# Performance work log

Measured on AMD Instinct MI355X. Metric: run time of the kernel, lower is better.

## Reference

```python
import jax, jax.numpy as jnp
import numpy as np

N, D_IN, D_HID, D_OUT, E = 8192, 1024, 4096, 1024, 8

def setup_inputs() -> dict:
    key = jax.random.key(0)
    ks = jax.random.split(key, 5)
    s_in = 1.0 / np.sqrt(D_IN)
    s_hid = 1.0 / np.sqrt(D_HID)
    return {
        "x": jax.random.normal(ks[0], (N, D_IN), dtype=jnp.float32),
        "W1": jax.random.normal(ks[1], (E, D_IN, D_HID), dtype=jnp.float32) * s_in,
        "b1": jnp.zeros((E, D_HID), dtype=jnp.float32),
        "W2": jax.random.normal(ks[2], (E, D_HID, D_OUT), dtype=jnp.float32) * s_hid,
        "b2": jnp.zeros((E, D_OUT), dtype=jnp.float32),
        "Wg": jax.random.normal(ks[3], (D_IN, E), dtype=jnp.float32) * s_in,
        "bg": jnp.zeros((E,), dtype=jnp.float32),
        "k": 2,
    }

def reference(x, W1, b1, W2, b2, Wg, bg, k):
    # Gating: softmax over ALL experts, then mask to top-k and renormalize
    scores = x @ Wg + bg                      # [N, E]
    _, topk_idx = jax.lax.top_k(scores, k)    # [N, k]
    mask = jax.nn.one_hot(topk_idx, scores.shape[-1], dtype=scores.dtype).sum(-2)  # [N, E]
    w = jax.nn.softmax(scores, axis=-1) * mask
    w = w / (w.sum(-1, keepdims=True) + 1e-8)  # [N, E]
    # Dense compute-all-experts (faithful to torch.stack over experts)
    h = jax.nn.relu(jnp.einsum('ni,eih->enh', x, W1) + b1[:, None, :])  # [E, N, hid]
    outs = jnp.einsum('enh,eho->eno', h, W2) + b2[:, None, :]           # [E, N, out]
    # Weighted combine over experts
    return jnp.einsum('ne,eno->no', w, outs)   # [N, out]
```

## Files before the change

kernel.cpp:

```cpp
#include <hip/hip_runtime.h>
#include <hip/hip_bf16.h>
#include <stdint.h>

#define N_TOK 8192
#define DIN   1024
#define DHID  4096
#define DOUT  1024
#define NE    8

typedef __attribute__((ext_vector_type(8))) __bf16 bf16x8;
typedef __attribute__((ext_vector_type(4))) float  f32x4;
typedef __attribute__((ext_vector_type(8))) unsigned short u16x8;

__device__ __forceinline__ unsigned short f2bfu(float f) {
    union { float f; unsigned u; } a; a.f = f;
    unsigned r = a.u + 0x7FFF + ((a.u >> 16) & 1);
    return (unsigned short)(r >> 16);
}

__device__ __forceinline__ void gload_lds16(const void* g, void* l) {
    __builtin_amdgcn_global_load_lds(
        (__attribute__((address_space(1))) void*)(void*)g,
        (__attribute__((address_space(3))) void*)l,
        16, 0, 0);
}

__global__ void transpose_cast_kernel(const float* __restrict__ in, unsigned short* __restrict__ out,
                                      int R, int C) {
    __shared__ float t[64][65];
    const size_t RC = (size_t)R * C;
    const float* ine = in + (size_t)blockIdx.z * RC;
    unsigned short* oute = out + (size_t)blockIdx.z * RC;
    int c0 = blockIdx.x * 64, r0 = blockIdx.y * 64;
    int tid = threadIdx.x;
    #pragma unroll
    for (int it = 0; it < 4; it++) {
        int idx = it * 256 + tid;
        int r = idx >> 4, cq = (idx & 15) * 4;
        float4 v = *(const float4*)(ine + (size_t)(r0 + r) * C + c0 + cq);
        t[r][cq] = v.x; t[r][cq + 1] = v.y; t[r][cq + 2] = v.z; t[r][cq + 3] = v.w;
    }
    __syncthreads();
    #pragma unroll
    for (int it = 0; it < 2; it++) {
        int u = it * 256 + tid;
        int c = u >> 3, g = (u & 7) * 8;
        u16x8 o;
        #pragma unroll
        for (int v = 0; v < 8; v++) o[v] = f2bfu(t[g + v][c]);
        *(u16x8*)(oute + (size_t)(c0 + c) * R + r0 + g) = o;
    }
}

__global__ void gate_kernel(const float* __restrict__ x, const float* __restrict__ Wg,
                            const float* __restrict__ bg, int* __restrict__ counts,
                            int* __restrict__ tok_list, int* __restrict__ slot_list,
                            float* __restrict__ wslot, unsigned short* __restrict__ xb) {
    int wv = threadIdx.x >> 6, lane = threadIdx.x & 63;
    int n = blockIdx.x * 4 + wv;
    float acc[NE];
    #pragma unroll
    for (int e = 0; e < NE; e++) acc[e] = 0.f;
    const float* xr = x + (size_t)n * DIN;
    unsigned short* xbr = xb + (size_t)n * DIN;
    #pragma unroll
    for (int i = 0; i < DIN / 256; i++) {
        int d = i * 256 + lane * 4;
        float4 xv = *(const float4*)(xr + d);
        ushort4 o;
        o.x = f2bfu(xv.x); o.y = f2bfu(xv.y); o.z = f2bfu(xv.z); o.w = f2bfu(xv.w);
        *(ushort4*)(xbr + d) = o;
        const float* w = Wg + (size_t)d * NE;
        #pragma unroll
        for (int u = 0; u < 4; u++) {
            float xs = (&xv.x)[u];
            float4 w0 = *(const float4*)(w + u * NE);
            float4 w1 = *(const float4*)(w + u * NE + 4);
            acc[0] += xs * w0.x; acc[1] += xs * w0.y; acc[2] += xs * w0.z; acc[3] += xs * w0.w;
            acc[4] += xs * w1.x; acc[5] += xs * w1.y; acc[6] += xs * w1.z; acc[7] += xs * w1.w;
        }
    }
    #pragma unroll
    for (int off = 32; off; off >>= 1)
        #pragma unroll
        for (int e = 0; e < NE; e++) acc[e] += __shfl_down(acc[e], off);
    if (lane == 0) {
        float s[NE], p[NE];
        float mx = -1e30f;
        #pragma unroll
        for (int e = 0; e < NE; e++) { s[e] = acc[e] + bg[e]; mx = fmaxf(mx, s[e]); }
        float sum = 0.f;
        #pragma unroll
        for (int e = 0; e < NE; e++) { p[e] = expf(s[e] - mx); sum += p[e]; }
        float inv = 1.f / sum;
        int e0 = 0;
        #pragma unroll
        for (int e = 1; e < NE; e++) if (s[e] > s[e0]) e0 = e;
        int e1 = (e0 == 0) ? 1 : 0;
        #pragma unroll
        for (int e = 0; e < NE; e++) if (e != e0 && s[e] > s[e1]) e1 = e;
        float p0 = p[e0] * inv, p1 = p[e1] * inv;
        float rn = 1.f / (p0 + p1 + 1e-8f);
        int pos0 = atomicAdd(&counts[e0], 1);
        tok_list[e0 * N_TOK + pos0] = n; slot_list[e0 * N_TOK + pos0] = 2 * n;     wslot[e0 * N_TOK + pos0] = p0 * rn;
        int pos1 = atomicAdd(&counts[e1], 1);
        tok_list[e1 * N_TOK + pos1] = n; slot_list[e1 * N_TOK + pos1] = 2 * n + 1; wslot[e1 * N_TOK + pos1] = p1 * rn;
    }
}

template <int KDIM, int NDIM, bool IS_GEMM1, int SPLITK>
__global__ __launch_bounds__(256, 4)
void moe_gemm(const unsigned short* __restrict__ Asrc, const unsigned short* __restrict__ Bt,
              const float* __restrict__ bias, unsigned short* __restrict__ Hdst,
              float* __restrict__ Odst, const int* __restrict__ counts,
              const int* __restrict__ tok_list, const int* __restrict__ slot_list,
              const float* __restrict__ wslot) {
    constexpr int NT_N = NDIM / 128;
    constexpr int NT_M = N_TOK / 128;
    constexpr int KLEN = KDIM / SPLITK;

    int e = blockIdx.x & 7;
    int local = blockIdx.x >> 3;
    int count = counts[e];

    __shared__ __align__(16) unsigned short As[128 * 64];
    __shared__ __align__(16) unsigned short Bs[128 * 64];
    __shared__ int rowid_s[128];
    __shared__ int outid_s[128];
    __shared__ float w_s[128];

    int tid = threadIdx.x;
    int lane = tid & 63;
    int wv = tid >> 6;
    int ric = lane >> 3;
    int k8  = (lane & 7) ^ ric;
    int wm = (wv >> 1) * 64, wn = (wv & 1) * 64;
    int r16 = lane & 15, quad = lane >> 4;

    for (int w = local; ; w += 128) {
        int tile_n = w % NT_N;
        int r = w / NT_N;
        int kh = r % SPLITK;
        int tile_m = r / SPLITK;
        if (tile_m >= NT_M) break;
        if (tile_m * 128 >= count) break;

        __syncthreads();
        if (tid < 128) {
            int rr = tile_m * 128 + tid;
            if (rr >= count) rr = tile_m * 128;
            int base = e * N_TOK + rr;
            if (IS_GEMM1) { rowid_s[tid] = tok_list[base]; outid_s[tid] = slot_list[base]; }
            else          { rowid_s[tid] = slot_list[base]; outid_s[tid] = tok_list[base]; w_s[tid] = wslot[base]; }
        }
        __syncthreads();

        const int k0 = kh * KLEN;
        const unsigned short* aptr[4];
        const unsigned short* bptr[4];
        #pragma unroll
        for (int i = 0; i < 4; i++) {
            int c = wv * 4 + i;
            int row = c * 8 + ric;
            aptr[i] = Asrc + (size_t)rowid_s[row] * KDIM + k0 + k8 * 8;
            bptr[i] = Bt + ((size_t)e * NDIM + tile_n * 128 + row) * KDIM + k0 + k8 * 8;
        }

        f32x4 acc[4][4];
        #pragma unroll
        for (int i = 0; i < 4; i++)
            #pragma unroll
            for (int j = 0; j < 4; j++) acc[i][j] = (f32x4){0.f, 0.f, 0.f, 0.f};

        for (int kk = 0; kk < KLEN / 64; kk++) {
            #pragma unroll
            for (int i = 0; i < 4; i++) {
                gload_lds16(aptr[i] + kk * 64, (void*)(As + (wv * 4 + i) * 512));
                gload_lds16(bptr[i] + kk * 64, (void*)(Bs + (wv * 4 + i) * 512));
            }
            __syncthreads();
            #pragma unroll
            for (int kh2 = 0; kh2 < 2; kh2++) {
                int swk = ((kh2 * 4 + quad) ^ (r16 & 7)) * 8;
                bf16x8 av[4], bv[4];
                #pragma unroll
                for (int i = 0; i < 4; i++)
                    av[i] = *(const bf16x8*)(As + (wm + i * 16 + r16) * 64 + swk);
                #pragma unroll
                for (int j = 0; j < 4; j++)
                    bv[j] = *(const bf16x8*)(Bs + (wn + j * 16 + r16) * 64 + swk);
                #pragma unroll
                for (int i = 0; i < 4; i++)
                    #pragma unroll
                    for (int j = 0; j < 4; j++)
                        acc[i][j] = __builtin_amdgcn_mfma_f32_16x16x32_bf16(av[i], bv[j], acc[i][j], 0, 0, 0);
            }
            __syncthreads();
        }

        float bias_r[4];
        #pragma unroll
        for (int j = 0; j < 4; j++)
            bias_r[j] = bias[(size_t)e * NDIM + tile_n * 128 + wn + j * 16 + r16];
        #pragma unroll
        for (int i = 0; i < 4; i++) {
            #pragma unroll
            for (int reg = 0; reg < 4; reg++) {
                int rr = wm + i * 16 + quad * 4 + reg;
                if (tile_m * 128 + rr >= count) continue;
                #pragma unroll
                for (int j = 0; j < 4; j++) {
                    int col = tile_n * 128 + wn + j * 16 + r16;
                    float v = acc[i][j][reg];
                    if (IS_GEMM1) {
                        v = fmaxf(v + bias_r[j], 0.f);
                        Hdst[(size_t)outid_s[rr] * NDIM + col] = f2bfu(v);
                    } else {
                        if (kh == 0) v += bias_r[j];
                        atomicAdd(&Odst[(size_t)outid_s[rr] * NDIM + col], w_s[rr] * v);
                    }
                }
            }
        }
    }
}

extern "C" void kernel_launch(void* const* d_in, const int* in_sizes, int n_in,
                              void* d_out, int out_size, void* d_ws, size_t ws_size,
                              hipStream_t stream) {
    const float* x  = (const float*)d_in[0];
    const float* W1 = (const float*)d_in[1];
    const float* b1 = (const float*)d_in[2];
    const float* W2 = (const float*)d_in[3];
    const float* b2 = (const float*)d_in[4];
    const float* Wg = (const float*)d_in[5];
    const float* bg = (const float*)d_in[6];
    float* out = (float*)d_out;

    char* ws = (char*)d_ws;
    unsigned short* xb  = (unsigned short*)(ws + 0);
    unsigned short* w1t = (unsigned short*)(ws + 16777216);
    unsigned short* w2t = (unsigned short*)(ws + 83886080);
    unsigned short* h   = (unsigned short*)(ws + 150994944);
    int*   counts    = (int*)(ws + 285212672);
    int*   tok_list  = (int*)(ws + 285212928);
    int*   slot_list = (int*)(ws + 285475072);
    float* wslot     = (float*)(ws + 285737216);

    hipMemsetAsync(counts, 0, 256, stream);
    hipMemsetAsync(d_out, 0, (size_t)out_size * sizeof(float), stream);

    transpose_cast_kernel<<<dim3(DHID / 64, DIN / 64, NE), 256, 0, stream>>>(W1, w1t, DIN, DHID);
    transpose_cast_kernel<<<dim3(DOUT / 64, DHID / 64, NE), 256, 0, stream>>>(W2, w2t, DHID, DOUT);
    gate_kernel<<<N_TOK / 4, 256, 0, stream>>>(x, Wg, bg, counts, tok_list, slot_list, wslot, xb);

    moe_gemm<DIN, DHID, true, 1><<<1024, 256, 0, stream>>>(
        xb, w1t, b1, h, nullptr, counts, tok_list, slot_list, wslot);
    moe_gemm<DHID, DOUT, false, 2><<<1024, 256, 0, stream>>>(
        h, w2t, b2, nullptr, out, counts, tok_list, slot_list, wslot);
}
```

Baseline: 881.4 us.

## Use 256x256 tiles with 8-wave double-buffered LDS pipeline in MoE GEMMs

Rewrites both grouped MoE GEMMs to use 256x256 output tiles computed by 512-thread blocks. The blocks use double-buffered dynamic LDS filled by global_load_lds, explicit vmcnt/lgkmcnt waits and barriers, and s_setprio around the MFMA clusters. The goal is to overlap global-to-LDS loads with MFMA work and raise arithmetic intensity per LDS byte. The grid shrinks to 256 persistent blocks that each loop over a per-expert work list, and GEMM2 split-K goes from 2 to 4 so there are enough work items. Risks include lower occupancy (one large block per CU), more atomics in the second GEMM, and load imbalance across experts with coarser tiles.

```diff
diff --git a/kernel.cpp b/kernel.cpp
--- a/kernel.cpp
+++ b/kernel.cpp
@@ -24,6 +24,12 @@
         (__attribute__((address_space(3))) void*)l,
         16, 0, 0);
 }
+
+#define SBAR()   asm volatile("s_barrier" ::: "memory")
+#define LGKM0()  do { asm volatile("s_waitcnt lgkmcnt(0)" ::: "memory"); \
+                      __builtin_amdgcn_sched_barrier(0); } while (0)
+#define VMCNT4() asm volatile("s_waitcnt vmcnt(4)" ::: "memory")
+#define VMCNT0() asm volatile("s_waitcnt vmcnt(0)" ::: "memory")
 
 __global__ void transpose_cast_kernel(const float* __restrict__ in, unsigned short* __restrict__ out,
                                       int R, int C) {
@@ -108,120 +114,213 @@
     }
 }
 
+__device__ __forceinline__ void rd4(bf16x8 (&dst)[4][2], const unsigned short* base,
+                                    const int (&row0)[4], const int (&ko)[2]) {
+    #pragma unroll
+    for (int f = 0; f < 4; f++)
+        #pragma unroll
+        for (int ks = 0; ks < 2; ks++)
+            dst[f][ks] = *(const bf16x8*)(base + row0[f] + ko[ks]);
+}
+__device__ __forceinline__ void rd2(bf16x8 (&dst)[2][2], const unsigned short* base,
+                                    const int (&row0)[2], const int (&ko)[2]) {
+    #pragma unroll
+    for (int f = 0; f < 2; f++)
+        #pragma unroll
+        for (int ks = 0; ks < 2; ks++)
+            dst[f][ks] = *(const bf16x8*)(base + row0[f] + ko[ks]);
+}
+template <int MH, int NH>
+__device__ __forceinline__ void mfq(f32x4 (&acc)[2][4][2][2], const bf16x8 (&av)[4][2],
+                                    const bf16x8 (&bv)[2][2]) {
+    #pragma unroll
+    for (int mf = 0; mf < 4; mf++)
+        #pragma unroll
+        for (int nf = 0; nf < 2; nf++)
+            #pragma unroll
+            for (int ks = 0; ks < 2; ks++)
+                acc[MH][mf][NH][nf] = __builtin_amdgcn_mfma_f32_16x16x32_bf16(
+                    av[mf][ks], bv[nf][ks], acc[MH][mf][NH][nf], 0, 0, 0);
+}
+
 template <int KDIM, int NDIM, bool IS_GEMM1, int SPLITK>
-__global__ __launch_bounds__(256, 4)
+__global__ __launch_bounds__(512, 2)
 void moe_gemm(const unsigned short* __restrict__ Asrc, const unsigned short* __restrict__ Bt,
               const float* __restrict__ bias, unsigned short* __restrict__ Hdst,
               float* __restrict__ Odst, const int* __restrict__ counts,
               const int* __restrict__ tok_list, const int* __restrict__ slot_list,
               const float* __restrict__ wslot) {
-    constexpr int NT_N = NDIM / 128;
-    constexpr int NT_M = N_TOK / 128;
+    constexpr int NT_N = NDIM / 256;
     constexpr int KLEN = KDIM / SPLITK;
-
-    int e = blockIdx.x & 7;
-    int local = blockIdx.x >> 3;
-    int count = counts[e];
-
-    __shared__ __align__(16) unsigned short As[128 * 64];
-    __shared__ __align__(16) unsigned short Bs[128 * 64];
-    __shared__ int rowid_s[128];
-    __shared__ int outid_s[128];
-    __shared__ float w_s[128];
-
-    int tid = threadIdx.x;
-    int lane = tid & 63;
-    int wv = tid >> 6;
-    int ric = lane >> 3;
-    int k8  = (lane & 7) ^ ric;
-    int wm = (wv >> 1) * 64, wn = (wv & 1) * 64;
-    int r16 = lane & 15, quad = lane >> 4;
-
-    for (int w = local; ; w += 128) {
-        int tile_n = w % NT_N;
-        int r = w / NT_N;
-        int kh = r % SPLITK;
-        int tile_m = r / SPLITK;
-        if (tile_m >= NT_M) break;
-        if (tile_m * 128 >= count) break;
+    constexpr int NKT  = KLEN / 64;
+    static_assert((NKT & 1) == 0 && NKT >= 4, "pipeline needs even NKT >= 4");
+
+    extern __shared__ char smem[];
+    unsigned short* As = (unsigned short*)smem;
+    unsigned short* Bs = (unsigned short*)(smem + 65536);
+    int*   rowid_s = (int*)(smem + 131072);
+    int*   outid_s = (int*)(smem + 132096);
+    float* w_s     = (float*)(smem + 133120);
+
+    const int e = blockIdx.x & 7;
+    const int local = blockIdx.x >> 3;
+    const int count = counts[e];
+    const int Mt = (count + 255) >> 8;
+    const int items = NT_N * SPLITK * Mt;
+
+    const int tid = threadIdx.x;
+    const int lane = tid & 63;
+    const int wv = tid >> 6;
+    const int wm2 = (wv >> 2) * 64;
+    const int wn2 = (wv & 3) * 32;
+    const int r16 = lane & 15, quad = lane >> 4;
+    const int lr = lane >> 3, ls = lane & 7;
+    const int ksrc8 = (ls ^ lr) * 8;
+
+    int arow0[4], brow0[2], koff[2];
+    #pragma unroll
+    for (int mf = 0; mf < 4; mf++) arow0[mf] = (wm2 + mf * 16 + r16) * 64;
+    #pragma unroll
+    for (int nf = 0; nf < 2; nf++) brow0[nf] = (wn2 + nf * 16 + r16) * 64;
+    #pragma unroll
+    for (int ks = 0; ks < 2; ks++) koff[ks] = ((ks * 4 + quad) ^ (r16 & 7)) * 8;
+
+    const char* Abase = (const char*)Asrc;
+    const char* Bbase = (const char*)(Bt + (size_t)e * NDIM * KDIM);
+
+    for (int w_it = local; w_it < items; w_it += 32) {
+        int tile_m = w_it % Mt;
+        int rdec = w_it / Mt;
+        int tile_n = rdec % NT_N;
+        int kh = rdec / NT_N;
+        const int k0 = kh * KLEN;
 
         __syncthreads();
-        if (tid < 128) {
-            int rr = tile_m * 128 + tid;
-            if (rr >= count) rr = tile_m * 128;
+        if (tid < 256) {
+            int rr = tile_m * 256 + tid;
+            if (rr >= count) rr = tile_m * 256;
             int base = e * N_TOK + rr;
             if (IS_GEMM1) { rowid_s[tid] = tok_list[base]; outid_s[tid] = slot_list[base]; }
             else          { rowid_s[tid] = slot_list[base]; outid_s[tid] = tok_list[base]; w_s[tid] = wslot[base]; }
         }
         __syncthreads();
 
-        const int k0 = kh * KLEN;
-        const unsigned short* aptr[4];
-        const unsigned short* bptr[4];
-        #pragma unroll
-        for (int i = 0; i < 4; i++) {
-            int c = wv * 4 + i;
-            int row = c * 8 + ric;
-            aptr[i] = Asrc + (size_t)rowid_s[row] * KDIM + k0 + k8 * 8;
-            bptr[i] = Bt + ((size_t)e * NDIM + tile_n * 128 + row) * KDIM + k0 + k8 * 8;
+        uint32_t aoff[2][2], boff[2][2];
+        #pragma unroll
+        for (int h = 0; h < 2; h++)
+            #pragma unroll
+            for (int g = 0; g < 2; g++) {
+                int rla = h * 128 + (wv * 2 + g) * 8 + lr;
+                aoff[h][g] = (uint32_t)rowid_s[rla] * (uint32_t)(KDIM * 2) + (uint32_t)(k0 + ksrc8) * 2u;
+                boff[h][g] = (uint32_t)(tile_n * 256 + rla) * (uint32_t)(KDIM * 2) + (uint32_t)(k0 + ksrc8) * 2u;
+            }
+
+#define STAGE_A(t2, h) do {                                                        \
+        unsigned short* _d = As + (((t2) & 1) * 16384) + (h) * 8192 + wv * 1024;   \
+        gload_lds16(Abase + aoff[h][0] + (size_t)(t2) * 128, (void*)_d);           \
+        gload_lds16(Abase + aoff[h][1] + (size_t)(t2) * 128, (void*)(_d + 512));   \
+    } while (0)
+#define STAGE_B(t2, h) do {                                                        \
+        unsigned short* _d = Bs + (((t2) & 1) * 16384) + (h) * 8192 + wv * 1024;   \
+        gload_lds16(Bbase + boff[h][0] + (size_t)(t2) * 128, (void*)_d);           \
+        gload_lds16(Bbase + boff[h][1] + (size_t)(t2) * 128, (void*)(_d + 512));   \
+    } while (0)
+#define RDA(buf, Mh) rd4(av, As + (buf) * 16384 + (Mh) * 8192, arow0, koff)
+#define RDB(buf, Nh) rd2(bv, Bs + (buf) * 16384 + (Nh) * 8192, brow0, koff)
+
+        f32x4 acc[2][4][2][2];
+        #pragma unroll
+        for (int a0 = 0; a0 < 2; a0++)
+            #pragma unroll
+            for (int a1 = 0; a1 < 4; a1++)
+                #pragma unroll
+                for (int a2 = 0; a2 < 2; a2++)
+                    #pragma unroll
+                    for (int a3 = 0; a3 < 2; a3++)
+                        acc[a0][a1][a2][a3] = (f32x4){0.f, 0.f, 0.f, 0.f};
+
+        bf16x8 av[4][2], bv[2][2];
+
+        STAGE_A(0, 0); STAGE_A(0, 1); STAGE_B(0, 0); STAGE_B(0, 1);
+        STAGE_B(1, 0); STAGE_A(1, 1);
+        VMCNT4();
+        SBAR();
+
+#define TILE_BODY(t, buf) do {                                                     \
+                                                        \
+        RDA(buf, 0); RDB(buf, 0);                                                  \
+        if ((t) + 1 < NKT) STAGE_A((t) + 1, 0);                                    \
+        SBAR(); LGKM0();                                                           \
+        __builtin_amdgcn_s_setprio(1); mfq<0, 0>(acc, av, bv);                     \
+        __builtin_amdgcn_s_setprio(0);                                             \
+        SBAR();                                                                    \
+                                                      \
+        RDA(buf, 1);                                                               \
+        if ((t) + 1 < NKT) STAGE_B((t) + 1, 1);                                    \
+        SBAR(); LGKM0();                                                           \
+        __builtin_amdgcn_s_setprio(1); mfq<1, 0>(acc, av, bv);                     \
+        __builtin_amdgcn_s_setprio(0);                                             \
+        SBAR();                                                                    \
+                   \
+        RDB(buf, 1);                                                               \
+        if ((t) + 2 < NKT) STAGE_B((t) + 2, 0);                                    \
+        SBAR(); LGKM0();                                                           \
+        __builtin_amdgcn_s_setprio(1); mfq<1, 1>(acc, av, bv);                     \
+        __builtin_amdgcn_s_setprio(0);                                             \
+        SBAR();                                                                    \
+                                      \
+        RDA(buf, 0);                                                               \
+        if ((t) + 2 < NKT) STAGE_A((t) + 2, 1);                                    \
+        SBAR(); LGKM0();                                                           \
+        __builtin_amdgcn_s_setprio(1); mfq<0, 1>(acc, av, bv);                     \
+        __builtin_amdgcn_s_setprio(0);                                             \
+        if ((t) + 2 < NKT) { VMCNT4(); } else { VMCNT0(); }                        \
+        SBAR();                                                                    \
+    } while (0)
+
+        #pragma unroll 1
+        for (int tt = 0; tt < NKT; tt += 2) {
+            TILE_BODY(tt, 0);
+            TILE_BODY(tt + 1, 1);
         }
-
-        f32x4 acc[4][4];
-        #pragma unroll
-        for (int i = 0; i < 4; i++)
-            #pragma unroll
-            for (int j = 0; j < 4; j++) acc[i][j] = (f32x4){0.f, 0.f, 0.f, 0.f};
-
-        for (int kk = 0; kk < KLEN / 64; kk++) {
-            #pragma unroll
-            for (int i = 0; i < 4; i++) {
-                gload_lds16(aptr[i] + kk * 64, (void*)(As + (wv * 4 + i) * 512));
-                gload_lds16(bptr[i] + kk * 64, (void*)(Bs + (wv * 4 + i) * 512));
-            }
-            __syncthreads();
-            #pragma unroll
-            for (int kh2 = 0; kh2 < 2; kh2++) {
-                int swk = ((kh2 * 4 + quad) ^ (r16 & 7)) * 8;
-                bf16x8 av[4], bv[4];
+#undef TILE_BODY
+#undef STAGE_A
+#undef STAGE_B
+#undef RDA
+#undef RDB
+
+        float bias_r[2][2];
+        #pragma unroll
+        for (int Nh = 0; Nh < 2; Nh++)
+            #pragma unroll
+            for (int nf = 0; nf < 2; nf++)
+                bias_r[Nh][nf] = bias[(size_t)e * NDIM + tile_n * 256 + Nh * 128 + wn2 + nf * 16 + r16];
+
+        #pragma unroll
+        for (int Mh = 0; Mh < 2; Mh++)
+            #pragma unroll
+            for (int mf = 0; mf < 4; mf++)
                 #pragma unroll
-                for (int i = 0; i < 4; i++)
-                    av[i] = *(const bf16x8*)(As + (wm + i * 16 + r16) * 64 + swk);
-                #pragma unroll
-                for (int j = 0; j < 4; j++)
-                    bv[j] = *(const bf16x8*)(Bs + (wn + j * 16 + r16) * 64 + swk);
-                #pragma unroll
-                for (int i = 0; i < 4; i++)
+                for (int reg = 0; reg < 4; reg++) {
+                    int rr = Mh * 128 + wm2 + mf * 16 + quad * 4 + reg;
+                    if (tile_m * 256 + rr >= count) continue;
+                    int orow = outid_s[rr];
+                    float wr = IS_GEMM1 ? 0.f : w_s[rr];
                     #pragma unroll
-                    for (int j = 0; j < 4; j++)
-                        acc[i][j] = __builtin_amdgcn_mfma_f32_16x16x32_bf16(av[i], bv[j], acc[i][j], 0, 0, 0);
-            }
-            __syncthreads();
-        }
-
-        float bias_r[4];
-        #pragma unroll
-        for (int j = 0; j < 4; j++)
-            bias_r[j] = bias[(size_t)e * NDIM + tile_n * 128 + wn + j * 16 + r16];
-        #pragma unroll
-        for (int i = 0; i < 4; i++) {
-            #pragma unroll
-            for (int reg = 0; reg < 4; reg++) {
-                int rr = wm + i * 16 + quad * 4 + reg;
-                if (tile_m * 128 + rr >= count) continue;
-                #pragma unroll
-                for (int j = 0; j < 4; j++) {
-                    int col = tile_n * 128 + wn + j * 16 + r16;
-                    float v = acc[i][j][reg];
-                    if (IS_GEMM1) {
-                        v = fmaxf(v + bias_r[j], 0.f);
-                        Hdst[(size_t)outid_s[rr] * NDIM + col] = f2bfu(v);
-                    } else {
-                        if (kh == 0) v += bias_r[j];
-                        atomicAdd(&Odst[(size_t)outid_s[rr] * NDIM + col], w_s[rr] * v);
-                    }
+                    for (int Nh = 0; Nh < 2; Nh++)
+                        #pragma unroll
+                        for (int nf = 0; nf < 2; nf++) {
+                            int col = tile_n * 256 + Nh * 128 + wn2 + nf * 16 + r16;
+                            float v = acc[Mh][mf][Nh][nf][reg];
+                            if (IS_GEMM1) {
+                                v = fmaxf(v + bias_r[Nh][nf], 0.f);
+                                Hdst[(size_t)orow * NDIM + col] = f2bfu(v);
+                            } else {
+                                if (kh == 0) v += bias_r[Nh][nf];
+                                atomicAdd(&Odst[(size_t)orow * NDIM + col], wr * v);
+                            }
+                        }
                 }
-            }
-        }
     }
 }
 
@@ -247,6 +346,16 @@
     int*   slot_list = (int*)(ws + 285475072);
     float* wslot     = (float*)(ws + 285737216);
 
+    constexpr int SMEM_BYTES = 134144;
+    static bool s_init = []() {
+        hipFuncSetAttribute(reinterpret_cast<const void*>(&moe_gemm<DIN, DHID, true, 1>),
+                            hipFuncAttributeMaxDynamicSharedMemorySize, SMEM_BYTES);
+        hipFuncSetAttribute(reinterpret_cast<const void*>(&moe_gemm<DHID, DOUT, false, 4>),
+                            hipFuncAttributeMaxDynamicSharedMemorySize, SMEM_BYTES);
+        return true;
+    }();
+    (void)s_init;
+
     hipMemsetAsync(counts, 0, 256, stream);
     hipMemsetAsync(d_out, 0, (size_t)out_size * sizeof(float), stream);
 
@@ -254,8 +363,8 @@
     transpose_cast_kernel<<<dim3(DOUT / 64, DHID / 64, NE), 256, 0, stream>>>(W2, w2t, DHID, DOUT);
     gate_kernel<<<N_TOK / 4, 256, 0, stream>>>(x, Wg, bg, counts, tok_list, slot_list, wslot, xb);
 
-    moe_gemm<DIN, DHID, true, 1><<<1024, 256, 0, stream>>>(
+    moe_gemm<DIN, DHID, true, 1><<<256, 512, SMEM_BYTES, stream>>>(
         xb, w1t, b1, h, nullptr, counts, tok_list, slot_list, wslot);
-    moe_gemm<DHID, DOUT, false, 2><<<1024, 256, 0, stream>>>(
+    moe_gemm<DHID, DOUT, false, 4><<<256, 512, SMEM_BYTES, stream>>>(
         h, w2t, b2, nullptr, out, counts, tok_list, slot_list, wslot);
 }
```

New measurement: 1.066 ms. +20.9%, slower.

## Fuse weight transpose-casts into gate and first GEMM kernels

Applied to the files above, without the earlier changes.

Removes the two standalone transpose/cast kernels. The W1 transpose-cast now runs inside the gate kernel, with each of its 2048 blocks converting four tiles. The W2 transpose-cast runs inside the first expert GEMM, with each block converting eight tiles after its first work tile, reusing the GEMM's shared-memory pool. This saves two kernel launches and lets the weight conversion overlap with gating and GEMM1 compute. The cost is extra per-block work and longer tails in both kernels, plus possible register or occupancy pressure in the GEMM.

```diff
diff --git a/kernel.cpp b/kernel.cpp
--- a/kernel.cpp
+++ b/kernel.cpp
@@ -25,14 +25,16 @@
         16, 0, 0);
 }
 
-__global__ void transpose_cast_kernel(const float* __restrict__ in, unsigned short* __restrict__ out,
-                                      int R, int C) {
-    __shared__ float t[64][65];
+__device__ __forceinline__ void transpose_tile(const float* __restrict__ in,
+                                               unsigned short* __restrict__ out,
+                                               int R, int C, int bx, int by, int bz,
+                                               float (*t)[65]) {
     const size_t RC = (size_t)R * C;
-    const float* ine = in + (size_t)blockIdx.z * RC;
-    unsigned short* oute = out + (size_t)blockIdx.z * RC;
-    int c0 = blockIdx.x * 64, r0 = blockIdx.y * 64;
+    const float* ine = in + (size_t)bz * RC;
+    unsigned short* oute = out + (size_t)bz * RC;
+    int c0 = bx * 64, r0 = by * 64;
     int tid = threadIdx.x;
+    __syncthreads();
     #pragma unroll
     for (int it = 0; it < 4; it++) {
         int idx = it * 256 + tid;
@@ -55,7 +57,9 @@
 __global__ void gate_kernel(const float* __restrict__ x, const float* __restrict__ Wg,
                             const float* __restrict__ bg, int* __restrict__ counts,
                             int* __restrict__ tok_list, int* __restrict__ slot_list,
-                            float* __restrict__ wslot, unsigned short* __restrict__ xb) {
+                            float* __restrict__ wslot, unsigned short* __restrict__ xb,
+                            const float* __restrict__ W1, unsigned short* __restrict__ w1t) {
+    __shared__ float tg[64][65];
     int wv = threadIdx.x >> 6, lane = threadIdx.x & 63;
     int n = blockIdx.x * 4 + wv;
     float acc[NE];
@@ -106,6 +110,12 @@
         int pos1 = atomicAdd(&counts[e1], 1);
         tok_list[e1 * N_TOK + pos1] = n; slot_list[e1 * N_TOK + pos1] = 2 * n + 1; wslot[e1 * N_TOK + pos1] = p1 * rn;
     }
+    #pragma unroll 1
+    for (int j = 0; j < 4; j++) {
+        int id = blockIdx.x * 4 + j;
+        int bx = id & 63, by = (id >> 6) & 15, bz = id >> 10;
+        transpose_tile(W1, w1t, DIN, DHID, bx, by, bz, tg);
+    }
 }
 
 template <int KDIM, int NDIM, bool IS_GEMM1, int SPLITK>
@@ -114,7 +124,8 @@
               const float* __restrict__ bias, unsigned short* __restrict__ Hdst,
               float* __restrict__ Odst, const int* __restrict__ counts,
               const int* __restrict__ tok_list, const int* __restrict__ slot_list,
-              const float* __restrict__ wslot) {
+              const float* __restrict__ wslot,
+              const float* __restrict__ W2src, unsigned short* __restrict__ w2t_dst) {
     constexpr int NT_N = NDIM / 128;
     constexpr int NT_M = N_TOK / 128;
     constexpr int KLEN = KDIM / SPLITK;
@@ -123,8 +134,9 @@
     int local = blockIdx.x >> 3;
     int count = counts[e];
 
-    __shared__ __align__(16) unsigned short As[128 * 64];
-    __shared__ __align__(16) unsigned short Bs[128 * 64];
+    __shared__ __align__(16) unsigned short pool[2 * 128 * 64];
+    unsigned short* As = pool;
+    unsigned short* Bs = pool + 128 * 64;
     __shared__ int rowid_s[128];
     __shared__ int outid_s[128];
     __shared__ float w_s[128];
@@ -136,6 +148,8 @@
     int k8  = (lane & 7) ^ ric;
     int wm = (wv >> 1) * 64, wn = (wv & 1) * 64;
     int r16 = lane & 15, quad = lane >> 4;
+
+    bool tdone = !IS_GEMM1;
 
     for (int w = local; ; w += 128) {
         int tile_n = w % NT_N;
@@ -222,6 +236,31 @@
                 }
             }
         }
+
+        if constexpr (IS_GEMM1) {
+            if (!tdone) {
+                tdone = true;
+                float (*t)[65] = (float(*)[65])pool;
+                #pragma unroll 1
+                for (int j = 0; j < 8; j++) {
+                    int id = blockIdx.x * 8 + j;
+                    int bx = id & 15, by = (id >> 4) & 63, bz = id >> 10;
+                    transpose_tile(W2src, w2t_dst, DHID, DOUT, bx, by, bz, t);
+                }
+            }
+        }
+    }
+
+    if constexpr (IS_GEMM1) {
+        if (!tdone) {
+            float (*t)[65] = (float(*)[65])pool;
+            #pragma unroll 1
+            for (int j = 0; j < 8; j++) {
+                int id = blockIdx.x * 8 + j;
+                int bx = id & 15, by = (id >> 4) & 63, bz = id >> 10;
+                transpose_tile(W2src, w2t_dst, DHID, DOUT, bx, by, bz, t);
+            }
+        }
     }
 }
 
@@ -250,12 +289,11 @@
     hipMemsetAsync(counts, 0, 256, stream);
     hipMemsetAsync(d_out, 0, (size_t)out_size * sizeof(float), stream);
 
-    transpose_cast_kernel<<<dim3(DHID / 64, DIN / 64, NE), 256, 0, stream>>>(W1, w1t, DIN, DHID);
-    transpose_cast_kernel<<<dim3(DOUT / 64, DHID / 64, NE), 256, 0, stream>>>(W2, w2t, DHID, DOUT);
-    gate_kernel<<<N_TOK / 4, 256, 0, stream>>>(x, Wg, bg, counts, tok_list, slot_list, wslot, xb);
+    gate_kernel<<<N_TOK / 4, 256, 0, stream>>>(x, Wg, bg, counts, tok_list, slot_list, wslot, xb,
+                                               W1, w1t);
 
     moe_gemm<DIN, DHID, true, 1><<<1024, 256, 0, stream>>>(
-        xb, w1t, b1, h, nullptr, counts, tok_list, slot_list, wslot);
+        xb, w1t, b1, h, nullptr, counts, tok_list, slot_list, wslot, W2, w2t);
     moe_gemm<DHID, DOUT, false, 2><<<1024, 256, 0, stream>>>(
-        h, w2t, b2, nullptr, out, counts, tok_list, slot_list, wslot);
-}
+        h, w2t, b2, nullptr, out, counts, tok_list, slot_list, wslot, nullptr, nullptr);
+}
```

After: 843.9 us. 4.3% less time.
